# Kernel tuning notes

Measured on AMD Instinct MI355X. Metric: run time of the kernel, lower is better.

The kernel has to match this reference:

```python
import jax, jax.numpy as jnp
import numpy as np

VOCAB = 50257
EMB = 1024
H = 1024
LAYERS = 2
B = 64
S = 512


def gru_cell(x, h, w_ih, w_hh, b_ih, b_hh):
    # PyTorch GRUCell math. x:[B,in], h:[B,H], w_ih:[3H,in], w_hh:[3H,H]
    gi = x @ w_ih.T + b_ih            # [B,3H]
    gh = h @ w_hh.T + b_hh            # [B,3H]
    i_r, i_z, i_n = jnp.split(gi, 3, axis=1)
    h_r, h_z, h_n = jnp.split(gh, 3, axis=1)
    r = jax.nn.sigmoid(i_r + h_r)
    z = jax.nn.sigmoid(i_z + h_z)
    n = jnp.tanh(i_n + r * h_n)
    return (1.0 - z) * n + z * h


def setup_inputs() -> dict:
    key = jax.random.key(0)
    ks = jax.random.split(key, 16)
    s = 0.02
    inp = {
        "input_step": jax.random.randint(ks[0], (1, B), 0, VOCAB),
        "last_hidden": jax.random.normal(ks[1], (LAYERS, B, H), jnp.float32),
        "encoder_outputs": jax.random.normal(ks[2], (S, B, H), jnp.float32),
        "emb_table": jax.random.normal(ks[3], (VOCAB, EMB), jnp.float32) * s,
        "w_ih0": jax.random.normal(ks[4], (3 * H, EMB), jnp.float32) * s,
        "w_hh0": jax.random.normal(ks[5], (3 * H, H), jnp.float32) * s,
        "b_ih0": jnp.zeros((3 * H,), jnp.float32),
        "b_hh0": jnp.zeros((3 * H,), jnp.float32),
        "w_ih1": jax.random.normal(ks[6], (3 * H, H), jnp.float32) * s,
        "w_hh1": jax.random.normal(ks[7], (3 * H, H), jnp.float32) * s,
        "b_ih1": jnp.zeros((3 * H,), jnp.float32),
        "b_hh1": jnp.zeros((3 * H,), jnp.float32),
        "concat_w": jax.random.normal(ks[8], (H, 2 * H), jnp.float32) * s,
        "concat_b": jnp.zeros((H,), jnp.float32),
        "out_w": jax.random.normal(ks[9], (VOCAB, H), jnp.float32) * s,
        "out_b": jnp.zeros((VOCAB,), jnp.float32),
    }
    return inp


def reference(input_step, last_hidden, encoder_outputs, emb_table,
              w_ih0, w_hh0, b_ih0, b_hh0, w_ih1, w_hh1, b_ih1, b_hh1,
              concat_w, concat_b, out_w, out_b):
    # embedding (dropout=0 / eval mode)
    x = emb_table[input_step[0]]                       # [B,EMB]
    # 2-layer GRU, single time step
    h0 = gru_cell(x, last_hidden[0], w_ih0, w_hh0, b_ih0, b_hh0)   # [B,H]
    h1 = gru_cell(h0, last_hidden[1], w_ih1, w_hh1, b_ih1, b_hh1)  # [B,H]
    rnn_output = h1                                    # [B,H]
    hidden = jnp.stack([h0, h1], axis=0)               # [LAYERS,B,H]
    # Luong dot attention: scores [S,B] -> softmax over S per batch
    scores = jnp.einsum('bh,sbh->bs', rnn_output, encoder_outputs)  # [B,S]
    attn = jax.nn.softmax(scores, axis=1)              # [B,S]
    context = jnp.einsum('bs,sbh->bh', attn, encoder_outputs)       # [B,H]
    concat_in = jnp.concatenate([rnn_output, context], axis=1)      # [B,2H]
    concat_out = jnp.tanh(concat_in @ concat_w.T + concat_b)        # [B,H]
    logits = concat_out @ out_w.T + out_b              # [B,VOCAB]
    output = jax.nn.softmax(logits, axis=1)
    return (output, hidden)
```

## Files before the change

kernel.cpp:

```cpp
#include <hip/hip_runtime.h>
#include <hip/hip_bf16.h>
#include <math.h>

#define VOCAB 50257
#define EMB   1024
#define HID   1024
#define BATCH 64
#define SEQ   512
#define LOGITS_LD 50304
#define SCH   16
#define NCHUNK (SEQ / SCH)
#define NSLAB 786

typedef __attribute__((ext_vector_type(8))) short bf16x8;
typedef __attribute__((ext_vector_type(4))) float f32x4;

__device__ inline short f2bf(float x) {
    __hip_bfloat16 h = __float2bfloat16(x);
    return *reinterpret_cast<short*>(&h);
}

__device__ inline bf16x8 cvt8(const float4& a, const float4& b) {
    bf16x8 r;
    r[0] = f2bf(a.x); r[1] = f2bf(a.y); r[2] = f2bf(a.z); r[3] = f2bf(a.w);
    r[4] = f2bf(b.x); r[5] = f2bf(b.y); r[6] = f2bf(b.z); r[7] = f2bf(b.w);
    return r;
}

struct Prob {
    const void*  A;
    const int*   gidx;
    const float* W;
    const float* bias;
    float*       C;
    int N, K, ldc;
};

template <int KSLEN, int ADD_BIAS, int A_BF16>
__global__ __launch_bounds__(128, 2) void gemm_k(Prob p0, Prob p1, Prob p2)
{
    Prob P = (blockIdx.y == 0) ? p0 : ((blockIdx.y == 1) ? p1 : p2);

    const int lane = threadIdx.x & 63;
    const int wv   = threadIdx.x >> 6;
    const int rowi = lane & 15;
    const int kgi  = lane >> 4;
    const int col  = blockIdx.x * 32 + wv * 16 + rowi;
    const int wcol = min(col, P.N - 1);
    const int kbase = blockIdx.z * KSLEN + kgi * 8;

    const float* wp = P.W + (size_t)wcol * P.K + kbase;

    const float*  af[4];
    const ushort* ah[4];
#pragma unroll
    for (int mt = 0; mt < 4; ++mt) {
        int r  = rowi + mt * 16;
        int ar = P.gidx ? P.gidx[r] : r;
        af[mt] = (const float*) P.A + (size_t)ar * P.K + kbase;
        ah[mt] = (const ushort*)P.A + (size_t)ar * P.K + kbase;
    }

    f32x4 acc[4] = {};

    float4 wa0, wb0, wa1, wb1;
    bf16x8 h0b[4], h1b[4];
    float4 f0a[4], f0b[4], f1a[4], f1b[4];

    wa0 = *(const float4*)(wp);
    wb0 = *(const float4*)(wp + 4);
#pragma unroll
    for (int mt = 0; mt < 4; ++mt) {
        if (A_BF16) h0b[mt] = *(const bf16x8*)(ah[mt]);
        else { f0a[mt] = *(const float4*)(af[mt]); f0b[mt] = *(const float4*)(af[mt] + 4); }
    }
    wa1 = *(const float4*)(wp + 32);
    wb1 = *(const float4*)(wp + 36);
#pragma unroll
    for (int mt = 0; mt < 4; ++mt) {
        if (A_BF16) h1b[mt] = *(const bf16x8*)(ah[mt] + 32);
        else { f1a[mt] = *(const float4*)(af[mt] + 32); f1b[mt] = *(const float4*)(af[mt] + 36); }
    }

#pragma unroll
    for (int ks = 0; ks < KSLEN; ks += 64) {
        {
            float4 nwa = {}, nwb = {};
            bf16x8 nh[4] = {};
            float4 nfa[4] = {}, nfb[4] = {};
            if (ks + 64 < KSLEN) {
                nwa = *(const float4*)(wp + ks + 64);
                nwb = *(const float4*)(wp + ks + 68);
#pragma unroll
                for (int mt = 0; mt < 4; ++mt) {
                    if (A_BF16) nh[mt] = *(const bf16x8*)(ah[mt] + ks + 64);
                    else { nfa[mt] = *(const float4*)(af[mt] + ks + 64);
                           nfb[mt] = *(const float4*)(af[mt] + ks + 68); }
                }
            }
            bf16x8 b = cvt8(wa0, wb0);
#pragma unroll
            for (int mt = 0; mt < 4; ++mt) {
                bf16x8 a;
                if (A_BF16) a = h0b[mt]; else a = cvt8(f0a[mt], f0b[mt]);
                acc[mt] = __builtin_amdgcn_mfma_f32_16x16x32_bf16(a, b, acc[mt], 0, 0, 0);
            }
            wa0 = nwa; wb0 = nwb;
#pragma unroll
            for (int mt = 0; mt < 4; ++mt) {
                if (A_BF16) h0b[mt] = nh[mt];
                else { f0a[mt] = nfa[mt]; f0b[mt] = nfb[mt]; }
            }
        }
        {
            float4 nwa = {}, nwb = {};
            bf16x8 nh[4] = {};
            float4 nfa[4] = {}, nfb[4] = {};
            if (ks + 96 < KSLEN) {
                nwa = *(const float4*)(wp + ks + 96);
                nwb = *(const float4*)(wp + ks + 100);
#pragma unroll
                for (int mt = 0; mt < 4; ++mt) {
                    if (A_BF16) nh[mt] = *(const bf16x8*)(ah[mt] + ks + 96);
                    else { nfa[mt] = *(const float4*)(af[mt] + ks + 96);
                           nfb[mt] = *(const float4*)(af[mt] + ks + 100); }
                }
            }
            bf16x8 b = cvt8(wa1, wb1);
#pragma unroll
            for (int mt = 0; mt < 4; ++mt) {
                bf16x8 a;
                if (A_BF16) a = h1b[mt]; else a = cvt8(f1a[mt], f1b[mt]);
                acc[mt] = __builtin_amdgcn_mfma_f32_16x16x32_bf16(a, b, acc[mt], 0, 0, 0);
            }
            wa1 = nwa; wb1 = nwb;
#pragma unroll
            for (int mt = 0; mt < 4; ++mt) {
                if (A_BF16) h1b[mt] = nh[mt];
                else { f1a[mt] = nfa[mt]; f1b[mt] = nfb[mt]; }
            }
        }
    }

    if (col < P.N) {
        float bv = ADD_BIAS ? P.bias[col] : 0.0f;
        float* C = P.C + (size_t)blockIdx.z * 64 * P.ldc;
#pragma unroll
        for (int mt = 0; mt < 4; ++mt)
#pragma unroll
            for (int r = 0; r < 4; ++r) {
                int row = mt * 16 + kgi * 4 + r;
                C[(size_t)row * P.ldc + col] = acc[mt][r] + bv;
            }
    }
}

__device__ __forceinline__ void issue_panel(const float* __restrict__ W, int r0,
                                            int p, int tid, float4 (&stg)[16])
{
#pragma unroll
    for (int i = 0; i < 16; ++i) {
        int grow = min(r0 + p * 16 + i, VOCAB - 1);
        stg[i] = *(const float4*)(W + (size_t)grow * 1024 + tid * 4);
    }
}

__device__ __forceinline__ void write_panel(ushort* buf, int tid,
                                            const float4 (&stg)[16])
{
#pragma unroll
    for (int i = 0; i < 16; ++i) {
        unsigned lo = (unsigned)(unsigned short)f2bf(stg[i].x) |
                      ((unsigned)(unsigned short)f2bf(stg[i].y) << 16);
        unsigned hi = (unsigned)(unsigned short)f2bf(stg[i].z) |
                      ((unsigned)(unsigned short)f2bf(stg[i].w) << 16);
        uint2 u = {lo, hi};
        *(uint2*)((char*)buf + i * 2048 + ((tid * 8) ^ ((i & 7) << 4))) = u;
    }
}

__global__ __launch_bounds__(256)
__attribute__((amdgpu_waves_per_eu(2, 2)))
void logits_panel_k(
    const ushort* __restrict__ co_bf, const float* __restrict__ W,
    const float* __restrict__ bias, float* __restrict__ logits,
    float* __restrict__ pmax, float* __restrict__ psum, int* __restrict__ ctr)
{
    __shared__ ushort wp_s[2][16 * 1024];
    __shared__ int slab_sh;

    const int tid  = threadIdx.x;
    const int lane = tid & 63;
    const int wv   = tid >> 6;
    const int rowi = lane & 15;
    const int kgi  = lane >> 4;
    const int wswz = (rowi & 7) << 4;

    bf16x8 cob[32];
    {
        const ushort* cp = co_bf + (size_t)(wv * 16 + rowi) * 1024 + kgi * 8;
#pragma unroll
        for (int s = 0; s < 32; ++s)
            cob[s] = *(const bf16x8*)(cp + s * 32);
    }

    while (true) {
        if (tid == 0) slab_sh = atomicAdd(ctr, 1);
        __syncthreads();
        const int slab = slab_sh;
        __syncthreads();
        if (slab >= NSLAB) break;
        const int r0 = slab * 64;

        float4 stg[16];

        issue_panel(W, r0, 0, tid, stg);
        write_panel(wp_s[0], tid, stg);
        issue_panel(W, r0, 1, tid, stg);
        asm volatile("s_waitcnt lgkmcnt(0)" ::: "memory");
        __builtin_amdgcn_s_barrier();

        float m_run = -INFINITY, s_run = 0.0f;

#pragma unroll
        for (int p = 0; p < 4; ++p) {
            f32x4 acc = {};
#pragma unroll
            for (int ks = 0; ks < 32; ++ks) {
                bf16x8 wf = *(const bf16x8*)((const char*)wp_s[p & 1] +
                            rowi * 2048 + ((ks * 64 + kgi * 16) ^ wswz));
                acc = __builtin_amdgcn_mfma_f32_16x16x32_bf16(wf, cob[ks], acc, 0, 0, 0);
            }

            const int vb = r0 + p * 16 + kgi * 4;
            const int bq = wv * 16 + rowi;
            float vals[4];
            if (vb + 3 < VOCAB) {
                float4 bv = *(const float4*)(bias + vb);
                vals[0] = acc[0] + bv.x; vals[1] = acc[1] + bv.y;
                vals[2] = acc[2] + bv.z; vals[3] = acc[3] + bv.w;
            } else {
#pragma unroll
                for (int r = 0; r < 4; ++r)
                    vals[r] = acc[r] + bias[min(vb + r, VOCAB - 1)];
            }
            float4 o = {vals[0], vals[1], vals[2], vals[3]};
            *(float4*)(logits + (size_t)bq * LOGITS_LD + vb) = o;

            float pmv = -INFINITY;
#pragma unroll
            for (int r = 0; r < 4; ++r)
                if (vb + r < VOCAB) pmv = fmaxf(pmv, vals[r]);
            pmv = fmaxf(pmv, __shfl_xor(pmv, 16));
            pmv = fmaxf(pmv, __shfl_xor(pmv, 32));
            float sp = 0.0f;
#pragma unroll
            for (int r = 0; r < 4; ++r)
                if (vb + r < VOCAB) sp += expf(vals[r] - pmv);
            sp += __shfl_xor(sp, 16);
            sp += __shfl_xor(sp, 32);
            float nm = fmaxf(m_run, pmv);
            s_run = s_run * expf(m_run - nm) +
                    ((pmv == -INFINITY) ? 0.0f : sp * expf(pmv - nm));
            m_run = nm;

            if (p < 3) {
                write_panel(wp_s[(p + 1) & 1], tid, stg);
                if (p < 2) issue_panel(W, r0, p + 2, tid, stg);
                asm volatile("s_waitcnt lgkmcnt(0)" ::: "memory");
                __builtin_amdgcn_s_barrier();
            }
        }

        if (kgi == 0) {
            pmax[(size_t)slab * 64 + wv * 16 + rowi] = m_run;
            psum[(size_t)slab * 64 + wv * 16 + rowi] = s_run;
        }
        __syncthreads();
    }
}

__global__ __launch_bounds__(256) void vfinal_k(
    const float* __restrict__ pmax, const float* __restrict__ psum,
    float* __restrict__ gm, float* __restrict__ ginv)
{
    const int b = blockIdx.x;
    __shared__ float red[4];
    float m = -INFINITY;
    for (int s = threadIdx.x; s < NSLAB; s += 256)
        m = fmaxf(m, pmax[(size_t)s * 64 + b]);
    for (int off = 32; off; off >>= 1) m = fmaxf(m, __shfl_xor(m, off));
    int wv = threadIdx.x >> 6, lane = threadIdx.x & 63;
    if (lane == 0) red[wv] = m;
    __syncthreads();
    m = fmaxf(fmaxf(red[0], red[1]), fmaxf(red[2], red[3]));
    float t = 0.0f;
    for (int s = threadIdx.x; s < NSLAB; s += 256)
        t += psum[(size_t)s * 64 + b] * expf(pmax[(size_t)s * 64 + b] - m);
    for (int off = 32; off; off >>= 1) t += __shfl_xor(t, off);
    __syncthreads();
    if (lane == 0) red[wv] = t;
    __syncthreads();
    if (threadIdx.x == 0) { gm[b] = m; ginv[b] = 1.0f / (red[0] + red[1] + red[2] + red[3]); }
}

template <int NZI, int NZH>
__global__ __launch_bounds__(256) void gru_gate_k(
    const float* __restrict__ pgi, const float* __restrict__ pgh,
    const float* __restrict__ b_ih, const float* __restrict__ b_hh,
    const float* __restrict__ hprev, float* __restrict__ out_hidden,
    float* __restrict__ h_out, float* __restrict__ ci)
{
    int i = blockIdx.x * 256 + threadIdx.x;
    int b = i >> 10, j = i & 1023;
    size_t base = (size_t)b * 3072 + j;
    float ir = b_ih[j], iz = b_ih[j + 1024], in_ = b_ih[j + 2048];
    float hr = b_hh[j], hz = b_hh[j + 1024], hn  = b_hh[j + 2048];
#pragma unroll
    for (int z = 0; z < NZI; ++z) {
        size_t o = (size_t)z * 64 * 3072 + base;
        ir += pgi[o]; iz += pgi[o + 1024]; in_ += pgi[o + 2048];
    }
#pragma unroll
    for (int z = 0; z < NZH; ++z) {
        size_t o = (size_t)z * 64 * 3072 + base;
        hr += pgh[o]; hz += pgh[o + 1024]; hn  += pgh[o + 2048];
    }
    float r = 1.0f / (1.0f + expf(-(ir + hr)));
    float z = 1.0f / (1.0f + expf(-(iz + hz)));
    float n = tanhf(in_ + r * hn);
    float v = (1.0f - z) * n + z * hprev[i];
    out_hidden[i] = v;
    if (h_out) h_out[i] = v;
    if (ci)    ci[(size_t)b * 2048 + j] = v;
}

__global__ __launch_bounds__(256) void attn_fused_k(
    const float* __restrict__ h1, const float* __restrict__ enc,
    float* __restrict__ pctx, float* __restrict__ pm, float* __restrict__ ps)
{
    const int b = blockIdx.y, ck = blockIdx.x;
    __shared__ float hs[HID];
    __shared__ float es[SCH][HID];
    __shared__ float sc[SCH];
    const int tid = threadIdx.x, wv = tid >> 6, lane = tid & 63;

    ((float4*)hs)[tid] = ((const float4*)(h1 + (size_t)b * HID))[tid];
    const float* ebase = enc + ((size_t)(ck * SCH) * BATCH + b) * HID;
#pragma unroll
    for (int i = 0; i < SCH; ++i) {
        int idx = tid + i * 256;
        int r = idx >> 8, c = idx & 255;
        ((float4*)es[r])[c] = ((const float4*)(ebase + (size_t)r * BATCH * HID))[c];
    }
    __syncthreads();

#pragma unroll
    for (int i = 0; i < 4; ++i) {
        int r = wv * 4 + i;
        float acc = 0.0f;
#pragma unroll
        for (int seg = 0; seg < 4; ++seg) {
            float4 ev = ((const float4*)es[r])[lane + seg * 64];
            float4 hv = ((const float4*)hs)[lane + seg * 64];
            acc += ev.x * hv.x + ev.y * hv.y + ev.z * hv.z + ev.w * hv.w;
        }
        for (int off = 32; off; off >>= 1) acc += __shfl_down(acc, off);
        if (lane == 0) sc[r] = acc;
    }
    __syncthreads();

    float m = sc[0];
#pragma unroll
    for (int s = 1; s < SCH; ++s) m = fmaxf(m, sc[s]);
    float p[SCH];
    float sum = 0.0f;
#pragma unroll
    for (int s = 0; s < SCH; ++s) { p[s] = expf(sc[s] - m); sum += p[s]; }

    float4 cacc = {0.0f, 0.0f, 0.0f, 0.0f};
#pragma unroll
    for (int s = 0; s < SCH; ++s) {
        float4 ev = ((const float4*)es[s])[tid];
        cacc.x += p[s] * ev.x; cacc.y += p[s] * ev.y;
        cacc.z += p[s] * ev.z; cacc.w += p[s] * ev.w;
    }
    ((float4*)(pctx + ((size_t)ck * BATCH + b) * HID))[tid] = cacc;
    if (tid == 0) { pm[b * NCHUNK + ck] = m; ps[b * NCHUNK + ck] = sum; }
}

__global__ __launch_bounds__(256) void attn_comb_k(
    const float* __restrict__ pctx, const float* __restrict__ pm,
    const float* __restrict__ ps, float* __restrict__ ci)
{
    const int b = blockIdx.x, tid = threadIdx.x;
    float m = -INFINITY;
#pragma unroll
    for (int c = 0; c < NCHUNK; ++c) m = fmaxf(m, pm[b * NCHUNK + c]);
    float w[NCHUNK]; float tot = 0.0f;
#pragma unroll
    for (int c = 0; c < NCHUNK; ++c) {
        w[c] = expf(pm[b * NCHUNK + c] - m);
        tot += ps[b * NCHUNK + c] * w[c];
    }
    float inv = 1.0f / tot;
    float4 acc = {0.0f, 0.0f, 0.0f, 0.0f};
#pragma unroll
    for (int c = 0; c < NCHUNK; ++c) {
        float4 v = ((const float4*)(pctx + ((size_t)c * BATCH + b) * HID))[tid];
        acc.x += w[c] * v.x; acc.y += w[c] * v.y;
        acc.z += w[c] * v.z; acc.w += w[c] * v.w;
    }
    float4 o = {acc.x * inv, acc.y * inv, acc.z * inv, acc.w * inv};
    ((float4*)(ci + (size_t)b * 2048 + 1024))[tid] = o;
}

__global__ __launch_bounds__(256) void concat_comb_k(
    const float* __restrict__ pco, const float* __restrict__ bias,
    ushort* __restrict__ co_bf, int* __restrict__ ctr)
{
    if (blockIdx.x == 0 && threadIdx.x == 0) *ctr = 0;
    int i = blockIdx.x * 256 + threadIdx.x;
    int j = i & 1023;
    float v = bias[j];
#pragma unroll
    for (int z = 0; z < 8; ++z) v += pco[(size_t)z * 65536 + i];
    co_bf[i] = (ushort)f2bf(tanhf(v));
}

__global__ __launch_bounds__(256) void softmax_v_k(
    const float* __restrict__ logits, const float* __restrict__ gm,
    const float* __restrict__ ginv, float* __restrict__ out)
{
    int b = blockIdx.y;
    float m = gm[b], inv = ginv[b];
    int v = blockIdx.x * 1024 + threadIdx.x * 4;
    if (v + 3 < VOCAB) {
        float4 lv = *reinterpret_cast<const float4*>(logits + (size_t)b * LOGITS_LD + v);
        float4 o;
        o.x = expf(lv.x - m) * inv; o.y = expf(lv.y - m) * inv;
        o.z = expf(lv.z - m) * inv; o.w = expf(lv.w - m) * inv;
        *reinterpret_cast<float4*>(out + (size_t)b * VOCAB + v) = o;
    } else {
        for (int k = 0; k < 4 && v + k < VOCAB; ++k)
            out[(size_t)b * VOCAB + v + k] = expf(logits[(size_t)b * LOGITS_LD + v + k] - m) * inv;
    }
}

extern "C" void kernel_launch(void* const* d_in, const int* in_sizes, int n_in,
                              void* d_out, int out_size, void* d_ws, size_t ws_size,
                              hipStream_t stream)
{
    const int*   input_step  = (const int*)  d_in[0];
    const float* last_hidden = (const float*)d_in[1];
    const float* enc         = (const float*)d_in[2];
    const float* emb         = (const float*)d_in[3];
    const float* w_ih0       = (const float*)d_in[4];
    const float* w_hh0       = (const float*)d_in[5];
    const float* b_ih0       = (const float*)d_in[6];
    const float* b_hh0       = (const float*)d_in[7];
    const float* w_ih1       = (const float*)d_in[8];
    const float* w_hh1       = (const float*)d_in[9];
    const float* b_ih1       = (const float*)d_in[10];
    const float* b_hh1       = (const float*)d_in[11];
    const float* concat_w    = (const float*)d_in[12];
    const float* concat_b    = (const float*)d_in[13];
    const float* out_w       = (const float*)d_in[14];
    const float* out_b       = (const float*)d_in[15];

    float* out = (float*)d_out;
    float* out_probs  = out;
    float* out_hidden = out + (size_t)BATCH * VOCAB;

    float* ws   = (float*)d_ws;
    float* big  = ws;
    float* pgi0 = big;
    float* pgh0 = big + 786432;
    float* pgh1 = big + 1572864;
    float* pgi1 = big;
    float* pctx = big;
    float* pco  = big;
    float* logits = ws + 2359296;
    float* ci   = logits + (size_t)64 * LOGITS_LD;
    float* h0   = ci + 131072;
    float* pm   = h0 + 65536;
    float* ps   = pm + 2048;
    float* pmax = ps + 2048;
    float* psum = pmax + 50304;
    float* gm   = psum + 50304;
    float* ginv = gm + 64;
    int*   ctr  = (int*)(ginv + 64);
    ushort* co_bf = (ushort*)(ginv + 64 + 16);

    Prob P0 = { emb,         input_step, w_ih0, nullptr, pgi0, 3 * HID, EMB, 3 * HID };
    Prob P1 = { last_hidden, nullptr,    w_hh0, nullptr, pgh0, 3 * HID, HID, 3 * HID };
    Prob P2 = { last_hidden + 64 * HID, nullptr, w_hh1, nullptr, pgh1, 3 * HID, HID, 3 * HID };

    gemm_k<256, 0, 0><<<dim3(96, 3, 4), 128, 0, stream>>>(P0, P1, P2);

    gru_gate_k<4, 4><<<256, 256, 0, stream>>>(pgi0, pgh0, b_ih0, b_hh0, last_hidden,
                                              out_hidden, h0, nullptr);

    Prob PB = { h0, nullptr, w_ih1, nullptr, pgi1, 3 * HID, HID, 3 * HID };
    gemm_k<128, 0, 0><<<dim3(96, 1, 8), 128, 0, stream>>>(PB, PB, PB);

    gru_gate_k<8, 4><<<256, 256, 0, stream>>>(pgi1, pgh1, b_ih1, b_hh1,
                                              last_hidden + 64 * HID,
                                              out_hidden + 64 * HID, nullptr, ci);

    attn_fused_k<<<dim3(NCHUNK, BATCH), 256, 0, stream>>>(
        out_hidden + 64 * HID, enc, pctx, pm, ps);
    attn_comb_k<<<BATCH, 256, 0, stream>>>(pctx, pm, ps, ci);

    Prob PC = { ci, nullptr, concat_w, nullptr, pco, HID, 2 * HID, HID };
    gemm_k<256, 0, 0><<<dim3(32, 1, 8), 128, 0, stream>>>(PC, PC, PC);
    concat_comb_k<<<256, 256, 0, stream>>>(pco, concat_b, co_bf, ctr);

    logits_panel_k<<<512, 256, 0, stream>>>(co_bf, out_w, out_b, logits, pmax, psum, ctr);

    vfinal_k<<<BATCH, 256, 0, stream>>>(pmax, psum, gm, ginv);
    softmax_v_k<<<dim3((VOCAB + 1023) / 1024, BATCH), 256, 0, stream>>>(
        logits, gm, ginv, out_probs);
}
```

Before: 173.1 us.

## Stream logits weights via direct global-to-LDS loads in a four-stage ring

The logits kernel stops staging fp32 weight rows through registers and converting them to bf16 before writing LDS. It now issues global_load_lds transfers straight into a four-slot fp32 LDS ring, keeping two chunks in flight and waiting on vmcnt. The bf16 conversion moves to read time, just before each MFMA. This is meant to remove register staging and conversion from the load path and deepen prefetch across a finer chunk schedule. The cost is extra per-MFMA conversion work, twice the LDS bytes per chunk, a barrier per chunk, and the end-of-slab __syncthreads is removed, which may leave a race on ring reuse across slabs.

```diff
diff --git a/kernel.cpp b/kernel.cpp
--- a/kernel.cpp
+++ b/kernel.cpp
@@ -15,6 +15,9 @@
 typedef __attribute__((ext_vector_type(8))) short bf16x8;
 typedef __attribute__((ext_vector_type(4))) float f32x4;
 
+typedef const __attribute__((address_space(1))) unsigned int gu32_t;
+typedef __attribute__((address_space(3))) unsigned int lu32_t;
+
 __device__ inline short f2bf(float x) {
     __hip_bfloat16 h = __float2bfloat16(x);
     return *reinterpret_cast<short*>(&h);
@@ -155,38 +158,14 @@
     }
 }
 
-__device__ __forceinline__ void issue_panel(const float* __restrict__ W, int r0,
-                                            int p, int tid, float4 (&stg)[16])
-{
-#pragma unroll
-    for (int i = 0; i < 16; ++i) {
-        int grow = min(r0 + p * 16 + i, VOCAB - 1);
-        stg[i] = *(const float4*)(W + (size_t)grow * 1024 + tid * 4);
-    }
-}
-
-__device__ __forceinline__ void write_panel(ushort* buf, int tid,
-                                            const float4 (&stg)[16])
-{
-#pragma unroll
-    for (int i = 0; i < 16; ++i) {
-        unsigned lo = (unsigned)(unsigned short)f2bf(stg[i].x) |
-                      ((unsigned)(unsigned short)f2bf(stg[i].y) << 16);
-        unsigned hi = (unsigned)(unsigned short)f2bf(stg[i].z) |
-                      ((unsigned)(unsigned short)f2bf(stg[i].w) << 16);
-        uint2 u = {lo, hi};
-        *(uint2*)((char*)buf + i * 2048 + ((tid * 8) ^ ((i & 7) << 4))) = u;
-    }
-}
-
 __global__ __launch_bounds__(256)
 __attribute__((amdgpu_waves_per_eu(2, 2)))
-void logits_panel_k(
+void logits_stream_k(
     const ushort* __restrict__ co_bf, const float* __restrict__ W,
     const float* __restrict__ bias, float* __restrict__ logits,
     float* __restrict__ pmax, float* __restrict__ psum, int* __restrict__ ctr)
 {
-    __shared__ ushort wp_s[2][16 * 1024];
+    __shared__ float wring[4][4096];
     __shared__ int slab_sh;
 
     const int tid  = threadIdx.x;
@@ -194,7 +173,11 @@
     const int wv   = tid >> 6;
     const int rowi = lane & 15;
     const int kgi  = lane >> 4;
-    const int wswz = (rowi & 7) << 4;
+
+    int soff[4];
+#pragma unroll
+    for (int j = 0; j < 4; ++j)
+        soff[j] = ((lane * 16) ^ (((wv * 4 + j) & 7) << 5)) >> 2;
 
     bf16x8 cob[32];
     {
@@ -203,6 +186,19 @@
         for (int s = 0; s < 32; ++s)
             cob[s] = *(const bf16x8*)(cp + s * 32);
     }
+    asm volatile("s_waitcnt vmcnt(0)" ::: "memory");
+
+#define ISSUE(c_) do {                                                        \
+        const int g_ = (c_) >> 2, q_ = (c_) & 3;                              \
+        _Pragma("unroll")                                                     \
+        for (int j = 0; j < 4; ++j) {                                         \
+            int r_ = wv * 4 + j;                                              \
+            int grow_ = min(r0 + g_ * 16 + r_, VOCAB - 1);                    \
+            __builtin_amdgcn_global_load_lds(                                 \
+                (gu32_t*)(W + (size_t)grow_ * 1024 + q_ * 256 + soff[j]),     \
+                (lu32_t*)&wring[(c_) & 3][r_ * 256], 16, 0, 0);               \
+        }                                                                     \
+    } while (0)
 
     while (true) {
         if (tid == 0) slab_sh = atomicAdd(ctr, 1);
@@ -212,63 +208,65 @@
         if (slab >= NSLAB) break;
         const int r0 = slab * 64;
 
-        float4 stg[16];
-
-        issue_panel(W, r0, 0, tid, stg);
-        write_panel(wp_s[0], tid, stg);
-        issue_panel(W, r0, 1, tid, stg);
-        asm volatile("s_waitcnt lgkmcnt(0)" ::: "memory");
-        __builtin_amdgcn_s_barrier();
+        ISSUE(0);
+        ISSUE(1);
 
         float m_run = -INFINITY, s_run = 0.0f;
-
-#pragma unroll
-        for (int p = 0; p < 4; ++p) {
-            f32x4 acc = {};
-#pragma unroll
-            for (int ks = 0; ks < 32; ++ks) {
-                bf16x8 wf = *(const bf16x8*)((const char*)wp_s[p & 1] +
-                            rowi * 2048 + ((ks * 64 + kgi * 16) ^ wswz));
-                acc = __builtin_amdgcn_mfma_f32_16x16x32_bf16(wf, cob[ks], acc, 0, 0, 0);
-            }
-
-            const int vb = r0 + p * 16 + kgi * 4;
-            const int bq = wv * 16 + rowi;
-            float vals[4];
-            if (vb + 3 < VOCAB) {
-                float4 bv = *(const float4*)(bias + vb);
-                vals[0] = acc[0] + bv.x; vals[1] = acc[1] + bv.y;
-                vals[2] = acc[2] + bv.z; vals[3] = acc[3] + bv.w;
-            } else {
+        f32x4 acc = {};
+
+#pragma unroll
+        for (int c = 0; c < 16; ++c) {
+            if (c + 2 < 16) ISSUE(c + 2);
+            if (c < 14)       asm volatile("s_waitcnt vmcnt(8)" ::: "memory");
+            else if (c == 14) asm volatile("s_waitcnt vmcnt(4)" ::: "memory");
+            else              asm volatile("s_waitcnt vmcnt(0)" ::: "memory");
+            __builtin_amdgcn_sched_barrier(0);
+            __builtin_amdgcn_s_barrier();
+
+            const char* cb = (const char*)&wring[c & 3][0] + rowi * 1024;
+#pragma unroll
+            for (int ks = 0; ks < 8; ++ks) {
+                int off = (ks * 128 + kgi * 32) ^ ((rowi & 7) << 5);
+                float4 fa = *(const float4*)(cb + off);
+                float4 fb = *(const float4*)(cb + off + 16);
+                acc = __builtin_amdgcn_mfma_f32_16x16x32_bf16(
+                    cvt8(fa, fb), cob[(c & 3) * 8 + ks], acc, 0, 0, 0);
+            }
+
+            if ((c & 3) == 3) {
+                const int g  = c >> 2;
+                const int vb = r0 + g * 16 + kgi * 4;
+                const int bq = wv * 16 + rowi;
+                float vals[4];
+                if (vb + 3 < VOCAB) {
+                    float4 bv = *(const float4*)(bias + vb);
+                    vals[0] = acc[0] + bv.x; vals[1] = acc[1] + bv.y;
+                    vals[2] = acc[2] + bv.z; vals[3] = acc[3] + bv.w;
+                } else {
+#pragma unroll
+                    for (int r = 0; r < 4; ++r)
+                        vals[r] = acc[r] + bias[min(vb + r, VOCAB - 1)];
+                }
+                float4 o = {vals[0], vals[1], vals[2], vals[3]};
+                *(float4*)(logits + (size_t)bq * LOGITS_LD + vb) = o;
+
+                float pmv = -INFINITY;
 #pragma unroll
                 for (int r = 0; r < 4; ++r)
-                    vals[r] = acc[r] + bias[min(vb + r, VOCAB - 1)];
-            }
-            float4 o = {vals[0], vals[1], vals[2], vals[3]};
-            *(float4*)(logits + (size_t)bq * LOGITS_LD + vb) = o;
-
-            float pmv = -INFINITY;
-#pragma unroll
-            for (int r = 0; r < 4; ++r)
-                if (vb + r < VOCAB) pmv = fmaxf(pmv, vals[r]);
-            pmv = fmaxf(pmv, __shfl_xor(pmv, 16));
-            pmv = fmaxf(pmv, __shfl_xor(pmv, 32));
-            float sp = 0.0f;
-#pragma unroll
-            for (int r = 0; r < 4; ++r)
-                if (vb + r < VOCAB) sp += expf(vals[r] - pmv);
-            sp += __shfl_xor(sp, 16);
-            sp += __shfl_xor(sp, 32);
-            float nm = fmaxf(m_run, pmv);
-            s_run = s_run * expf(m_run - nm) +
-                    ((pmv == -INFINITY) ? 0.0f : sp * expf(pmv - nm));
-            m_run = nm;
-
-            if (p < 3) {
-                write_panel(wp_s[(p + 1) & 1], tid, stg);
-                if (p < 2) issue_panel(W, r0, p + 2, tid, stg);
-                asm volatile("s_waitcnt lgkmcnt(0)" ::: "memory");
-                __builtin_amdgcn_s_barrier();
+                    if (vb + r < VOCAB) pmv = fmaxf(pmv, vals[r]);
+                pmv = fmaxf(pmv, __shfl_xor(pmv, 16));
+                pmv = fmaxf(pmv, __shfl_xor(pmv, 32));
+                float sp = 0.0f;
+#pragma unroll
+                for (int r = 0; r < 4; ++r)
+                    if (vb + r < VOCAB) sp += expf(vals[r] - pmv);
+                sp += __shfl_xor(sp, 16);
+                sp += __shfl_xor(sp, 32);
+                float nm = fmaxf(m_run, pmv);
+                s_run = s_run * expf(m_run - nm) +
+                        ((pmv == -INFINITY) ? 0.0f : sp * expf(pmv - nm));
+                m_run = nm;
+                acc = (f32x4){};
             }
         }
 
@@ -276,8 +274,8 @@
             pmax[(size_t)slab * 64 + wv * 16 + rowi] = m_run;
             psum[(size_t)slab * 64 + wv * 16 + rowi] = s_run;
         }
-        __syncthreads();
-    }
+    }
+#undef ISSUE
 }
 
 __global__ __launch_bounds__(256) void vfinal_k(
@@ -516,7 +514,8 @@
     gemm_k<256, 0, 0><<<dim3(32, 1, 8), 128, 0, stream>>>(PC, PC, PC);
     concat_comb_k<<<256, 256, 0, stream>>>(pco, concat_b, co_bf, ctr);
 
-    logits_panel_k<<<512, 256, 0, stream>>>(co_bf, out_w, out_b, logits, pmax, psum, ctr);
+    logits_stream_k<<<512, 256, 0, stream>>>(co_bf, out_w, out_b, logits,
+                                             pmax, psum, ctr);
 
     vfinal_k<<<BATCH, 256, 0, stream>>>(pmax, psum, gm, ginv);
     softmax_v_k<<<dim3((VOCAB + 1023) / 1024, BATCH), 256, 0, stream>>>(
```

Result: slower. 214.1 us (+23.6%).
